# Performance work log

Hardware: AMD Instinct MI355X
Metric: run time of the kernel (lower is better)

Reference implementation:

```python
import jax, jax.numpy as jnp
import numpy as np

B, IN, H, NC = 8192, 1024, 1024, 16
CS = H // NC  # chunk_size = 64


def cumsoftmax(x):
    # cumulative softmax along last dim
    return jnp.cumsum(jax.nn.softmax(x, axis=-1), axis=-1)


def setup_inputs() -> dict:
    key = jax.random.key(0)
    ks = jax.random.split(key, 9)
    s_ih = 1.0 / np.sqrt(IN)
    s_hh = 1.0 / np.sqrt(H)
    return {
        "x": jax.random.normal(ks[0], (B, IN), jnp.float32),
        "hx": jax.random.normal(ks[1], (B, H), jnp.float32),
        "cx": jax.random.normal(ks[2], (B, NC, CS), jnp.float32),
        "input_floor": jax.random.normal(ks[3], (B, NC), jnp.float32),
        "forget_floor": jax.random.normal(ks[4], (B, NC), jnp.float32),
        "W_ih": jax.random.uniform(ks[5], (4 * H, IN), jnp.float32, -s_ih, s_ih),
        "b_ih": jax.random.uniform(ks[6], (4 * H,), jnp.float32, -s_ih, s_ih),
        "W_hh": jax.random.uniform(ks[7], (4 * H, H), jnp.float32, -s_hh, s_hh),
        "b_hh": jax.random.uniform(ks[8], (4 * H,), jnp.float32, -s_hh, s_hh),
    }


def reference(x, hx, cx, input_floor, forget_floor, W_ih, b_ih, W_hh, b_hh):
    # dual GEMM (eval path: dropconnect=0.0 -> plain linear)
    gates = x @ W_ih.T + b_ih + hx @ W_hh.T + b_hh          # [B, 4H]
    g = gates.reshape(-1, NC * 4, CS)                        # [B, 4*NC, CS]
    outgate, cell, ingate, forgetgate = jnp.split(g, 4, axis=1)  # each [B, NC, CS]

    happy_in, sad_in = jnp.split(input_floor, 2, axis=1)     # [B, NC/2] each
    happy_fg, sad_fg = jnp.split(forget_floor, 2, axis=1)

    happy_cingate = cumsoftmax(happy_in)
    happy_cforgetgate = jnp.flip(cumsoftmax(jnp.flip(happy_fg, 1)), 1)
    sad_cingate = jnp.flip(cumsoftmax(jnp.flip(sad_in, 1)), 1)
    sad_cforgetgate = cumsoftmax(sad_fg)

    cingate = jnp.concatenate([happy_cingate, sad_cingate], axis=1)[:, :, None]      # [B, NC, 1]
    cforgetgate = jnp.concatenate([happy_cforgetgate, sad_cforgetgate], axis=1)[:, :, None]

    ingate = jax.nn.sigmoid(ingate)
    forgetgate = jax.nn.sigmoid(forgetgate)
    cell = jnp.tanh(cell)
    outgate = jax.nn.sigmoid(outgate)

    overlap = cforgetgate * cingate
    forgetgate = forgetgate * overlap + (cforgetgate - overlap)
    ingate = ingate * overlap + (cingate - overlap)

    cy = forgetgate * cx + ingate * cell                     # [B, NC, CS]
    hy = outgate * jnp.tanh(cy)
    return hy.reshape(-1, H), cy
```

## Files before the change

kernel.cpp:

```cpp
#include <hip/hip_runtime.h>
#include <hip/hip_bf16.h>


#define B_ROWS 8192
#define IN_DIM 1024
#define H_DIM  1024
#define NCHUNK 16
#define K_TOT  2048

#define BM   256
#define BN   256
#define BK   64
#define NKT  (K_TOT / BK)
#define THREADS 1024

#define A_PACK_BYTES ((size_t)B_ROWS * K_TOT * 2)
#define W_PACK_BYTES ((size_t)16 * 256 * K_TOT * 2)

typedef __attribute__((ext_vector_type(4))) float  f32x4;
typedef __bf16 bf16x8 __attribute__((ext_vector_type(8)));

__device__ __forceinline__ float sigmoidf_(float x) {
    return 1.0f / (1.0f + __expf(-x));
}
__device__ __forceinline__ float tanhf_(float x) {
    float e = __expf(-2.0f * fabsf(x));
    float t = (1.0f - e) / (1.0f + e);
    return copysignf(t, x);
}

__device__ __forceinline__ void gload16(const __bf16* gsrc, __bf16* lds_dst) {
    __builtin_amdgcn_global_load_lds(
        (const __attribute__((address_space(1))) unsigned int*)gsrc,
        (__attribute__((address_space(3))) unsigned int*)lds_dst, 16, 0, 0);
}

__device__ __forceinline__ bf16x8 cvt8(f32x4 v0, f32x4 v1) {
    bf16x8 o;
    o[0] = (__bf16)v0.x; o[1] = (__bf16)v0.y; o[2] = (__bf16)v0.z; o[3] = (__bf16)v0.w;
    o[4] = (__bf16)v1.x; o[5] = (__bf16)v1.y; o[6] = (__bf16)v1.z; o[7] = (__bf16)v1.w;
    return o;
}

__global__ __launch_bounds__(256)
void pack_AW(const float* __restrict__ x, const float* __restrict__ hx,
             const float* __restrict__ W_ih, const float* __restrict__ W_hh,
             __bf16* __restrict__ Abf, __bf16* __restrict__ Wp)
{
    const int bid = blockIdx.x;
    const int c8  = threadIdx.x << 3;
    if (bid < B_ROWS) {
        const float* src = (c8 < IN_DIM)
            ? (x  + (size_t)bid * IN_DIM + c8)
            : (hx + (size_t)bid * IN_DIM + (c8 - IN_DIM));
        f32x4 v0 = *reinterpret_cast<const f32x4*>(src);
        f32x4 v1 = *reinterpret_cast<const f32x4*>(src + 4);
        *reinterpret_cast<bf16x8*>(Abf + (size_t)bid * K_TOT + c8) = cvt8(v0, v1);
    } else {
        const int r  = bid - B_ROWS;
        const int bh = r >> 8;
        const int n  = r & 255;
        const int g  = (n >> 4) & 3;
        const int j  = (n >> 6) * 16 + (n & 15);
        const int wr = g * H_DIM + bh * 64 + j;
        const float* src = (c8 < IN_DIM)
            ? (W_ih + (size_t)wr * IN_DIM + c8)
            : (W_hh + (size_t)wr * IN_DIM + (c8 - IN_DIM));
        f32x4 v0 = *reinterpret_cast<const f32x4*>(src);
        f32x4 v1 = *reinterpret_cast<const f32x4*>(src + 4);
        *reinterpret_cast<bf16x8*>(Wp + (size_t)r * K_TOT + c8) = cvt8(v0, v1);
    }
}

__device__ __forceinline__ void stage_half(const __bf16* __restrict__ gbase, int kb,
                                           __bf16* lbase, int row0, int tid) {
    int e   = tid * 8;
    int row = row0 + (e >> 6);
    int kd  = e & 63;
    gload16(gbase + (size_t)row * K_TOT + kb + (kd ^ ((row & 7) << 3)), lbase + e);
}

#define SWZ(r, k) ((r) * 64 + ((k) ^ (((r) & 7) << 3)))

#define LDB(Bs) { \
    _Pragma("unroll") \
    for (int fn = 0; fn < 4; ++fn) { \
        int br = wcol + fn * 16 + lr; \
        bfr[fn][0] = *reinterpret_cast<const bf16x8*>(&(Bs)[SWZ(br, lh * 8)]); \
        bfr[fn][1] = *reinterpret_cast<const bf16x8*>(&(Bs)[SWZ(br, 32 + lh * 8)]); \
    } }

#define LDA(As, q) { \
    int ar = wrow + (q) * 16 + lr; \
    af[0] = *reinterpret_cast<const bf16x8*>(&(As)[SWZ(ar, lh * 8)]); \
    af[1] = *reinterpret_cast<const bf16x8*>(&(As)[SWZ(ar, 32 + lh * 8)]); \
    }

#define BARRIER do { \
    asm volatile("" ::: "memory"); \
    __builtin_amdgcn_s_barrier(); \
    asm volatile("" ::: "memory"); \
} while (0)

#define MF_Q(q) { \
    __builtin_amdgcn_s_setprio(1); \
    _Pragma("unroll") \
    for (int ks = 0; ks < 2; ++ks) { \
        _Pragma("unroll") \
        for (int fn = 0; fn < 4; ++fn) { \
            acc[q][fn] = __builtin_amdgcn_mfma_f32_16x16x32_bf16(af[ks], bfr[fn][ks], acc[q][fn], 0, 0, 0); \
        } \
    } \
    __builtin_amdgcn_s_setprio(0); \
}

#define TILE12(T, Ac, An, Bc) { \
    const int t_ = (T); \
     \
    LDB(Bc); \
    LDA(Ac, 0); \
    stage_half(Arow, ((t_ + 1) & 31) * BK, An,        0,   tid); \
    stage_half(Arow, ((t_ + 1) & 31) * BK, An + 8192, 128, tid); \
    MF_Q(0); \
    BARRIER; \
     \
    LDA(Ac, 1); \
    stage_half(Wblk, ((t_ + 2) & 31) * BK, Bc,        0,   tid); \
    MF_Q(1); \
     \
    LDA(Ac, 2); \
    stage_half(Wblk, ((t_ + 2) & 31) * BK, Bc + 8192, 128, tid); \
    MF_Q(2); \
     \
    LDA(Ac, 3); \
    MF_Q(3); \
    asm volatile("s_waitcnt lgkmcnt(0)" ::: "memory"); \
    asm volatile("s_waitcnt vmcnt(2)"   ::: "memory"); \
    BARRIER; \
}

__global__ __launch_bounds__(THREADS, 4)
void onlstm_gemm12(const __bf16* __restrict__ Abf, const __bf16* __restrict__ Wp,
                   const float* __restrict__ cx,
                   const float* __restrict__ input_floor,
                   const float* __restrict__ forget_floor,
                   const float* __restrict__ b_ih, const float* __restrict__ b_hh,
                   float* __restrict__ out)
{
    __shared__ __align__(16) __bf16 lds[65536];
    __shared__ float ci_s[BM], cf_s[BM], bias_s[BN];

    const int tid = threadIdx.x;
    const int n0  = blockIdx.x;
    const int bm  = (n0 & 7) * 4 + ((n0 >> 3) & 3);
    const int bh  = n0 >> 5;
    const int h0  = bh * 64;
    const int nc  = bh;

    if (tid < BM) {
        {
            int g = (tid >> 4) & 3;
            int j = (tid >> 6) * 16 + (tid & 15);
            int wrr = g * H_DIM + h0 + j;
            bias_s[tid] = b_ih[wrr] + b_hh[wrr];
        }
        int b = bm * BM + tid;
        const int off = (nc < 8) ? 0 : 8;
        const int ic  = (nc < 8) ? nc : (nc - 8);
        const float* pin = input_floor  + (size_t)b * NCHUNK + off;
        const float* pfg = forget_floor + (size_t)b * NCHUNK + off;
        float vi[8], vf[8];
        float mi = -1e30f, mf = -1e30f;
        #pragma unroll
        for (int t = 0; t < 8; ++t) {
            vi[t] = pin[t]; vf[t] = pfg[t];
            mi = fmaxf(mi, vi[t]); mf = fmaxf(mf, vf[t]);
        }
        float si = 0.f, sf = 0.f;
        #pragma unroll
        for (int t = 0; t < 8; ++t) {
            vi[t] = __expf(vi[t] - mi); vf[t] = __expf(vf[t] - mf);
            si += vi[t]; sf += vf[t];
        }
        float pi = 0.f, pf = 0.f;
        #pragma unroll
        for (int t = 0; t < 8; ++t) { if (t <= ic) { pi += vi[t]; pf += vf[t]; } }
        float suf_i = si - pi + vi[ic];
        float suf_f = sf - pf + vf[ic];
        float civ, cfv;
        if (nc < 8) { civ = pi / si;    cfv = suf_f / sf; }
        else        { civ = suf_i / si; cfv = pf / sf;    }
        ci_s[tid] = civ; cf_s[tid] = cfv;
    }

    const __bf16* Arow = Abf + (size_t)(bm * BM) * K_TOT;
    const __bf16* Wblk = Wp  + (size_t)bh * 256 * K_TOT;
    __bf16* const A0p = lds;
    __bf16* const A1p = lds + 16384;
    __bf16* const B0p = lds + 32768;
    __bf16* const B1p = lds + 49152;

    stage_half(Arow, 0,  A0p,        0,   tid);
    stage_half(Arow, 0,  A0p + 8192, 128, tid);
    stage_half(Wblk, 0,  B0p,        0,   tid);
    stage_half(Wblk, 0,  B0p + 8192, 128, tid);
    stage_half(Wblk, BK, B1p,        0,   tid);
    stage_half(Wblk, BK, B1p + 8192, 128, tid);
    asm volatile("s_waitcnt lgkmcnt(0)" ::: "memory");
    asm volatile("s_waitcnt vmcnt(2)"   ::: "memory");
    __builtin_amdgcn_s_barrier();
    asm volatile("" ::: "memory");

    f32x4  acc[4][4];
    #pragma unroll
    for (int i = 0; i < 4; ++i)
        #pragma unroll
        for (int j = 0; j < 4; ++j) acc[i][j] = (f32x4){0.f, 0.f, 0.f, 0.f};
    bf16x8 af[2];
    bf16x8 bfr[4][2];

    const int l    = tid & 63;
    const int wid  = tid >> 6;
    const int wrw  = wid >> 2;
    const int wc   = wid & 3;
    const int lr   = l & 15;
    const int lh   = l >> 4;
    const int wrow = wrw * 64;
    const int wcol = wc * 64;

    #pragma unroll 1
    for (int it = 0; it < NKT / 2; ++it) {
        const int t = 2 * it;
        TILE12(t,     A0p, A1p, B0p);
        TILE12(t + 1, A1p, A0p, B1p);
    }
    asm volatile("s_waitcnt vmcnt(0) lgkmcnt(0)" ::: "memory");

    const size_t CY_OFF = (size_t)B_ROWS * H_DIM;
    const int hcol = h0 + wc * 16 + lr;
    #pragma unroll
    for (int m = 0; m < 4; ++m) {
        #pragma unroll
        for (int r = 0; r < 4; ++r) {
            int rt = wrow + m * 16 + lh * 4 + r;
            int b  = bm * BM + rt;
            float civ = ci_s[rt], cfv = cf_s[rt];
            float ovl = cfv * civ;
            float og = acc[m][0][r] + bias_s[wcol + lr];
            float cg = acc[m][1][r] + bias_s[wcol + 16 + lr];
            float ig = acc[m][2][r] + bias_s[wcol + 32 + lr];
            float fg = acc[m][3][r] + bias_s[wcol + 48 + lr];
            float i_s = sigmoidf_(ig);
            float f_s = sigmoidf_(fg);
            float c_t = tanhf_(cg);
            float o_s = sigmoidf_(og);
            float fq = f_s * ovl + (cfv - ovl);
            float iq = i_s * ovl + (civ - ovl);
            float cxv = cx[(size_t)b * H_DIM + hcol];
            float cyv = fq * cxv + iq * c_t;
            float hyv = o_s * tanhf_(cyv);
            out[(size_t)b * H_DIM + hcol] = hyv;
            out[CY_OFF + (size_t)b * H_DIM + hcol] = cyv;
        }
    }
}

extern "C" void kernel_launch(void* const* d_in, const int* in_sizes, int n_in,
                              void* d_out, int out_size, void* d_ws, size_t ws_size,
                              hipStream_t stream) {
    const float* x            = (const float*)d_in[0];
    const float* hx           = (const float*)d_in[1];
    const float* cx           = (const float*)d_in[2];
    const float* input_floor  = (const float*)d_in[3];
    const float* forget_floor = (const float*)d_in[4];
    const float* W_ih         = (const float*)d_in[5];
    const float* b_ih         = (const float*)d_in[6];
    const float* W_hh         = (const float*)d_in[7];
    const float* b_hh         = (const float*)d_in[8];
    float* out = (float*)d_out;

    __bf16* Abf = (__bf16*)d_ws;
    __bf16* Wp  = (__bf16*)((char*)d_ws + A_PACK_BYTES);
    pack_AW<<<B_ROWS + 16 * 256, 256, 0, stream>>>(x, hx, W_ih, W_hh, Abf, Wp);
    onlstm_gemm12<<<512, THREADS, 0, stream>>>(
        Abf, Wp, cx, input_floor, forget_floor, b_ih, b_hh, out);
}
```

Before: 161.3 us.

## Shrink GEMM tile to 128x256 with single-buffered LDS and simple loop

Halves the M tile to 128 rows and the block to 512 threads, doubling the grid to 1024 blocks. The double-buffered, interleaved prefetch pipeline is replaced by a single LDS buffer with load, wait, barrier, compute each K step, and the MFMA priority hints are dropped. The aim is more blocks per CU and less LDS per block, so occupancy hides latency instead of the software pipeline. The cost is that global loads no longer overlap with MFMA inside a block, and each B tile is reloaded twice as often.

```diff
diff --git a/kernel.cpp b/kernel.cpp
--- a/kernel.cpp
+++ b/kernel.cpp
@@ -8,11 +8,11 @@
 #define NCHUNK 16
 #define K_TOT  2048
 
-#define BM   256
+#define BM   128
 #define BN   256
 #define BK   64
 #define NKT  (K_TOT / BK)
-#define THREADS 1024
+#define THREADS 512
 
 #define A_PACK_BYTES ((size_t)B_ROWS * K_TOT * 2)
 #define W_PACK_BYTES ((size_t)16 * 256 * K_TOT * 2)
@@ -72,8 +72,8 @@
     }
 }
 
-__device__ __forceinline__ void stage_half(const __bf16* __restrict__ gbase, int kb,
-                                           __bf16* lbase, int row0, int tid) {
+__device__ __forceinline__ void stage_q(const __bf16* __restrict__ gbase, int kb,
+                                        __bf16* lbase, int row0, int tid) {
     int e   = tid * 8;
     int row = row0 + (e >> 6);
     int kd  = e & 63;
@@ -103,7 +103,6 @@
 } while (0)
 
 #define MF_Q(q) { \
-    __builtin_amdgcn_s_setprio(1); \
     _Pragma("unroll") \
     for (int ks = 0; ks < 2; ++ks) { \
         _Pragma("unroll") \
@@ -111,59 +110,33 @@
             acc[q][fn] = __builtin_amdgcn_mfma_f32_16x16x32_bf16(af[ks], bfr[fn][ks], acc[q][fn], 0, 0, 0); \
         } \
     } \
-    __builtin_amdgcn_s_setprio(0); \
-}
-
-#define TILE12(T, Ac, An, Bc) { \
-    const int t_ = (T); \
-     \
-    LDB(Bc); \
-    LDA(Ac, 0); \
-    stage_half(Arow, ((t_ + 1) & 31) * BK, An,        0,   tid); \
-    stage_half(Arow, ((t_ + 1) & 31) * BK, An + 8192, 128, tid); \
-    MF_Q(0); \
-    BARRIER; \
-     \
-    LDA(Ac, 1); \
-    stage_half(Wblk, ((t_ + 2) & 31) * BK, Bc,        0,   tid); \
-    MF_Q(1); \
-     \
-    LDA(Ac, 2); \
-    stage_half(Wblk, ((t_ + 2) & 31) * BK, Bc + 8192, 128, tid); \
-    MF_Q(2); \
-     \
-    LDA(Ac, 3); \
-    MF_Q(3); \
-    asm volatile("s_waitcnt lgkmcnt(0)" ::: "memory"); \
-    asm volatile("s_waitcnt vmcnt(2)"   ::: "memory"); \
-    BARRIER; \
 }
 
 __global__ __launch_bounds__(THREADS, 4)
-void onlstm_gemm12(const __bf16* __restrict__ Abf, const __bf16* __restrict__ Wp,
+void onlstm_gemm13(const __bf16* __restrict__ Abf, const __bf16* __restrict__ Wp,
                    const float* __restrict__ cx,
                    const float* __restrict__ input_floor,
                    const float* __restrict__ forget_floor,
                    const float* __restrict__ b_ih, const float* __restrict__ b_hh,
                    float* __restrict__ out)
 {
-    __shared__ __align__(16) __bf16 lds[65536];
+    __shared__ __align__(16) __bf16 lds[24576];
     __shared__ float ci_s[BM], cf_s[BM], bias_s[BN];
 
     const int tid = threadIdx.x;
     const int n0  = blockIdx.x;
-    const int bm  = (n0 & 7) * 4 + ((n0 >> 3) & 3);
-    const int bh  = n0 >> 5;
+    const int bm  = (n0 & 7) * 8 + ((n0 >> 3) & 7);
+    const int bh  = n0 >> 6;
     const int h0  = bh * 64;
     const int nc  = bh;
 
+    if (tid < BN) {
+        int g = (tid >> 4) & 3;
+        int j = (tid >> 6) * 16 + (tid & 15);
+        int wrr = g * H_DIM + h0 + j;
+        bias_s[tid] = b_ih[wrr] + b_hh[wrr];
+    }
     if (tid < BM) {
-        {
-            int g = (tid >> 4) & 3;
-            int j = (tid >> 6) * 16 + (tid & 15);
-            int wrr = g * H_DIM + h0 + j;
-            bias_s[tid] = b_ih[wrr] + b_hh[wrr];
-        }
         int b = bm * BM + tid;
         const int off = (nc < 8) ? 0 : 8;
         const int ic  = (nc < 8) ? nc : (nc - 8);
@@ -195,29 +168,8 @@
 
     const __bf16* Arow = Abf + (size_t)(bm * BM) * K_TOT;
     const __bf16* Wblk = Wp  + (size_t)bh * 256 * K_TOT;
-    __bf16* const A0p = lds;
-    __bf16* const A1p = lds + 16384;
-    __bf16* const B0p = lds + 32768;
-    __bf16* const B1p = lds + 49152;
-
-    stage_half(Arow, 0,  A0p,        0,   tid);
-    stage_half(Arow, 0,  A0p + 8192, 128, tid);
-    stage_half(Wblk, 0,  B0p,        0,   tid);
-    stage_half(Wblk, 0,  B0p + 8192, 128, tid);
-    stage_half(Wblk, BK, B1p,        0,   tid);
-    stage_half(Wblk, BK, B1p + 8192, 128, tid);
-    asm volatile("s_waitcnt lgkmcnt(0)" ::: "memory");
-    asm volatile("s_waitcnt vmcnt(2)"   ::: "memory");
-    __builtin_amdgcn_s_barrier();
-    asm volatile("" ::: "memory");
-
-    f32x4  acc[4][4];
-    #pragma unroll
-    for (int i = 0; i < 4; ++i)
-        #pragma unroll
-        for (int j = 0; j < 4; ++j) acc[i][j] = (f32x4){0.f, 0.f, 0.f, 0.f};
-    bf16x8 af[2];
-    bf16x8 bfr[4][2];
+    __bf16* const Ap = lds;
+    __bf16* const Bp = lds + 8192;
 
     const int l    = tid & 63;
     const int wid  = tid >> 6;
@@ -228,13 +180,33 @@
     const int wrow = wrw * 64;
     const int wcol = wc * 64;
 
+    f32x4  acc[4][4];
+    #pragma unroll
+    for (int i = 0; i < 4; ++i)
+        #pragma unroll
+        for (int j = 0; j < 4; ++j) acc[i][j] = (f32x4){0.f, 0.f, 0.f, 0.f};
+    bf16x8 af[2];
+    bf16x8 bfr[4][2];
+
     #pragma unroll 1
-    for (int it = 0; it < NKT / 2; ++it) {
-        const int t = 2 * it;
-        TILE12(t,     A0p, A1p, B0p);
-        TILE12(t + 1, A1p, A0p, B1p);
-    }
-    asm volatile("s_waitcnt vmcnt(0) lgkmcnt(0)" ::: "memory");
+    for (int t = 0; t < NKT; ++t) {
+        const int kb = t * BK;
+        asm volatile("s_waitcnt lgkmcnt(0)" ::: "memory");
+        BARRIER;
+        stage_q(Arow, kb, Ap,         0,   tid);
+        stage_q(Arow, kb, Ap + 4096,  64,  tid);
+        stage_q(Wblk, kb, Bp,         0,   tid);
+        stage_q(Wblk, kb, Bp + 4096,  64,  tid);
+        stage_q(Wblk, kb, Bp + 8192,  128, tid);
+        stage_q(Wblk, kb, Bp + 12288, 192, tid);
+        asm volatile("s_waitcnt vmcnt(0)" ::: "memory");
+        BARRIER;
+        LDB(Bp);
+        LDA(Ap, 0); MF_Q(0);
+        LDA(Ap, 1); MF_Q(1);
+        LDA(Ap, 2); MF_Q(2);
+        LDA(Ap, 3); MF_Q(3);
+    }
 
     const size_t CY_OFF = (size_t)B_ROWS * H_DIM;
     const int hcol = h0 + wc * 16 + lr;
@@ -282,6 +254,6 @@
     __bf16* Abf = (__bf16*)d_ws;
     __bf16* Wp  = (__bf16*)((char*)d_ws + A_PACK_BYTES);
     pack_AW<<<B_ROWS + 16 * 256, 256, 0, stream>>>(x, hx, W_ih, W_hh, Abf, Wp);
-    onlstm_gemm12<<<512, THREADS, 0, stream>>>(
+    onlstm_gemm13<<<1024, THREADS, 0, stream>>>(
         Abf, Wp, cx, input_floor, forget_floor, b_ih, b_hh, out);
 }
```

Result: faster. 157.7 us (-2.3%).

## Shrink GEMM tile to 128x256 with BK=32 and 512-thread blocks

Applied to the files above, without the earlier changes.

Halves the M tile and the K step, drops to 512 threads (8 waves) per block, and launches 1024 blocks instead of 512. LDS use falls from 128KB to 48KB so more blocks can be resident per CU, and the finer grid should balance better across CUs. The cost is lower operand reuse per block, twice as many K iterations with barriers, and a narrower swizzle pattern that may raise LDS bank conflicts.

```diff
diff --git a/kernel.cpp b/kernel.cpp
--- a/kernel.cpp
+++ b/kernel.cpp
@@ -8,11 +8,11 @@
 #define NCHUNK 16
 #define K_TOT  2048
 
-#define BM   256
+#define BM   128
 #define BN   256
-#define BK   64
+#define BK   32
 #define NKT  (K_TOT / BK)
-#define THREADS 1024
+#define THREADS 512
 
 #define A_PACK_BYTES ((size_t)B_ROWS * K_TOT * 2)
 #define W_PACK_BYTES ((size_t)16 * 256 * K_TOT * 2)
@@ -72,28 +72,26 @@
     }
 }
 
-__device__ __forceinline__ void stage_half(const __bf16* __restrict__ gbase, int kb,
-                                           __bf16* lbase, int row0, int tid) {
+__device__ __forceinline__ void stage_s(const __bf16* __restrict__ gbase, int kb,
+                                        __bf16* lbase, int row0, int tid) {
     int e   = tid * 8;
-    int row = row0 + (e >> 6);
-    int kd  = e & 63;
-    gload16(gbase + (size_t)row * K_TOT + kb + (kd ^ ((row & 7) << 3)), lbase + e);
-}
-
-#define SWZ(r, k) ((r) * 64 + ((k) ^ (((r) & 7) << 3)))
+    int row = row0 + (e >> 5);
+    int kd  = e & 31;
+    gload16(gbase + (size_t)row * K_TOT + kb + (kd ^ ((row & 3) << 3)), lbase + e);
+}
+
+#define SWZ32(r, k) ((r) * 32 + ((k) ^ (((r) & 3) << 3)))
 
 #define LDB(Bs) { \
     _Pragma("unroll") \
     for (int fn = 0; fn < 4; ++fn) { \
         int br = wcol + fn * 16 + lr; \
-        bfr[fn][0] = *reinterpret_cast<const bf16x8*>(&(Bs)[SWZ(br, lh * 8)]); \
-        bfr[fn][1] = *reinterpret_cast<const bf16x8*>(&(Bs)[SWZ(br, 32 + lh * 8)]); \
+        bfr[fn] = *reinterpret_cast<const bf16x8*>(&(Bs)[SWZ32(br, lh * 8)]); \
     } }
 
-#define LDA(As, q) { \
-    int ar = wrow + (q) * 16 + lr; \
-    af[0] = *reinterpret_cast<const bf16x8*>(&(As)[SWZ(ar, lh * 8)]); \
-    af[1] = *reinterpret_cast<const bf16x8*>(&(As)[SWZ(ar, 32 + lh * 8)]); \
+#define LDA(As, m) { \
+    int ar = wrow + (m) * 16 + lr; \
+    af = *reinterpret_cast<const bf16x8*>(&(As)[SWZ32(ar, lh * 8)]); \
     }
 
 #define BARRIER do { \
@@ -101,69 +99,66 @@
     __builtin_amdgcn_s_barrier(); \
     asm volatile("" ::: "memory"); \
 } while (0)
-
-#define MF_Q(q) { \
+#define LGKM0 asm volatile("s_waitcnt lgkmcnt(0)" ::: "memory")
+
+#define MF_M(m) { \
     __builtin_amdgcn_s_setprio(1); \
     _Pragma("unroll") \
-    for (int ks = 0; ks < 2; ++ks) { \
-        _Pragma("unroll") \
-        for (int fn = 0; fn < 4; ++fn) { \
-            acc[q][fn] = __builtin_amdgcn_mfma_f32_16x16x32_bf16(af[ks], bfr[fn][ks], acc[q][fn], 0, 0, 0); \
-        } \
+    for (int fn = 0; fn < 4; ++fn) { \
+        acc[m][fn] = __builtin_amdgcn_mfma_f32_16x16x32_bf16(af, bfr[fn], acc[m][fn], 0, 0, 0); \
     } \
     __builtin_amdgcn_s_setprio(0); \
 }
 
-#define TILE12(T, Ac, An, Bc) { \
+#define TILE16(T, Ac, An, Bc) { \
     const int t_ = (T); \
      \
     LDB(Bc); \
     LDA(Ac, 0); \
-    stage_half(Arow, ((t_ + 1) & 31) * BK, An,        0,   tid); \
-    stage_half(Arow, ((t_ + 1) & 31) * BK, An + 8192, 128, tid); \
-    MF_Q(0); \
+    stage_s(Arow, ((t_ + 1) & 63) * BK, An, 0, tid); \
+    MF_M(0); \
     BARRIER; \
      \
     LDA(Ac, 1); \
-    stage_half(Wblk, ((t_ + 2) & 31) * BK, Bc,        0,   tid); \
-    MF_Q(1); \
+    stage_s(Wblk, ((t_ + 2) & 63) * BK, Bc,        0,   tid); \
+    MF_M(1); \
      \
     LDA(Ac, 2); \
-    stage_half(Wblk, ((t_ + 2) & 31) * BK, Bc + 8192, 128, tid); \
-    MF_Q(2); \
+    stage_s(Wblk, ((t_ + 2) & 63) * BK, Bc + 4096, 128, tid); \
+    MF_M(2); \
      \
     LDA(Ac, 3); \
-    MF_Q(3); \
-    asm volatile("s_waitcnt lgkmcnt(0)" ::: "memory"); \
-    asm volatile("s_waitcnt vmcnt(2)"   ::: "memory"); \
+    MF_M(3); \
+    LGKM0; \
+    asm volatile("s_waitcnt vmcnt(2)" ::: "memory"); \
     BARRIER; \
 }
 
 __global__ __launch_bounds__(THREADS, 4)
-void onlstm_gemm12(const __bf16* __restrict__ Abf, const __bf16* __restrict__ Wp,
+void onlstm_gemm16(const __bf16* __restrict__ Abf, const __bf16* __restrict__ Wp,
                    const float* __restrict__ cx,
                    const float* __restrict__ input_floor,
                    const float* __restrict__ forget_floor,
                    const float* __restrict__ b_ih, const float* __restrict__ b_hh,
                    float* __restrict__ out)
 {
-    __shared__ __align__(16) __bf16 lds[65536];
+    __shared__ __align__(16) __bf16 lds[24576];
     __shared__ float ci_s[BM], cf_s[BM], bias_s[BN];
 
     const int tid = threadIdx.x;
     const int n0  = blockIdx.x;
-    const int bm  = (n0 & 7) * 4 + ((n0 >> 3) & 3);
-    const int bh  = n0 >> 5;
+    const int bm  = (n0 & 7) * 8 + ((n0 >> 3) & 7);
+    const int bh  = n0 >> 6;
     const int h0  = bh * 64;
     const int nc  = bh;
 
+    if (tid < BN) {
+        int g = (tid >> 4) & 3;
+        int j = (tid >> 6) * 16 + (tid & 15);
+        int wrr = g * H_DIM + h0 + j;
+        bias_s[tid] = b_ih[wrr] + b_hh[wrr];
+    }
     if (tid < BM) {
-        {
-            int g = (tid >> 4) & 3;
-            int j = (tid >> 6) * 16 + (tid & 15);
-            int wrr = g * H_DIM + h0 + j;
-            bias_s[tid] = b_ih[wrr] + b_hh[wrr];
-        }
         int b = bm * BM + tid;
         const int off = (nc < 8) ? 0 : 8;
         const int ic  = (nc < 8) ? nc : (nc - 8);
@@ -196,28 +191,9 @@
     const __bf16* Arow = Abf + (size_t)(bm * BM) * K_TOT;
     const __bf16* Wblk = Wp  + (size_t)bh * 256 * K_TOT;
     __bf16* const A0p = lds;
-    __bf16* const A1p = lds + 16384;
-    __bf16* const B0p = lds + 32768;
-    __bf16* const B1p = lds + 49152;
-
-    stage_half(Arow, 0,  A0p,        0,   tid);
-    stage_half(Arow, 0,  A0p + 8192, 128, tid);
-    stage_half(Wblk, 0,  B0p,        0,   tid);
-    stage_half(Wblk, 0,  B0p + 8192, 128, tid);
-    stage_half(Wblk, BK, B1p,        0,   tid);
-    stage_half(Wblk, BK, B1p + 8192, 128, tid);
-    asm volatile("s_waitcnt lgkmcnt(0)" ::: "memory");
-    asm volatile("s_waitcnt vmcnt(2)"   ::: "memory");
-    __builtin_amdgcn_s_barrier();
-    asm volatile("" ::: "memory");
-
-    f32x4  acc[4][4];
-    #pragma unroll
-    for (int i = 0; i < 4; ++i)
-        #pragma unroll
-        for (int j = 0; j < 4; ++j) acc[i][j] = (f32x4){0.f, 0.f, 0.f, 0.f};
-    bf16x8 af[2];
-    bf16x8 bfr[4][2];
+    __bf16* const A1p = lds + 4096;
+    __bf16* const B0p = lds + 8192;
+    __bf16* const B1p = lds + 16384;
 
     const int l    = tid & 63;
     const int wid  = tid >> 6;
@@ -228,11 +204,29 @@
     const int wrow = wrw * 64;
     const int wcol = wc * 64;
 
+    stage_s(Arow, 0,  A0p,        0,   tid);
+    stage_s(Wblk, 0,  B0p,        0,   tid);
+    stage_s(Wblk, 0,  B0p + 4096, 128, tid);
+    stage_s(Wblk, BK, B1p,        0,   tid);
+    stage_s(Wblk, BK, B1p + 4096, 128, tid);
+    LGKM0;
+    asm volatile("s_waitcnt vmcnt(2)" ::: "memory");
+    __builtin_amdgcn_s_barrier();
+    asm volatile("" ::: "memory");
+
+    f32x4  acc[4][4];
+    #pragma unroll
+    for (int i = 0; i < 4; ++i)
+        #pragma unroll
+        for (int j = 0; j < 4; ++j) acc[i][j] = (f32x4){0.f, 0.f, 0.f, 0.f};
+    bf16x8 af;
+    bf16x8 bfr[4];
+
     #pragma unroll 1
     for (int it = 0; it < NKT / 2; ++it) {
         const int t = 2 * it;
-        TILE12(t,     A0p, A1p, B0p);
-        TILE12(t + 1, A1p, A0p, B1p);
+        TILE16(t,     A0p, A1p, B0p);
+        TILE16(t + 1, A1p, A0p, B1p);
     }
     asm volatile("s_waitcnt vmcnt(0) lgkmcnt(0)" ::: "memory");
 
@@ -282,6 +276,6 @@
     __bf16* Abf = (__bf16*)d_ws;
     __bf16* Wp  = (__bf16*)((char*)d_ws + A_PACK_BYTES);
     pack_AW<<<B_ROWS + 16 * 256, 256, 0, stream>>>(x, hx, W_ih, W_hh, Abf, Wp);
-    onlstm_gemm12<<<512, THREADS, 0, stream>>>(
+    onlstm_gemm16<<<1024, THREADS, 0, stream>>>(
         Abf, Wp, cx, input_floor, forget_floor, b_ih, b_hh, out);
 }
```

Result: slower. 193.7 us (+20.1%).
